# Performance work log

Measured on AMD Instinct MI355X. Metric: run time of the kernel, lower is better.

## Reference

```python
import jax, jax.numpy as jnp
import numpy as np

B, C, L = 16, 256, 2048

def setup_inputs() -> dict:
    key = jax.random.key(0)
    y = jax.random.normal(key, (B, C, L), dtype=jnp.float32)
    alpha = jnp.float32(0.5)
    beta = jnp.float32(0.5)
    gamma = jnp.float32(0.0)
    return {"y": y, "alpha": alpha, "beta": beta, "gamma": gamma}

def reference(y, alpha, beta, gamma):
    # y: [B, C, L]
    Bs, Cs, Ls = y.shape
    # channel attention: scores over channels, scaled by 1/sqrt(L)
    scale_c = 1.0 / np.sqrt(max(Ls, 1)).astype(np.float32)
    scores_c = jnp.einsum('bcl,bdl->bcd', y, y) * scale_c          # [B, C, C]
    attn_c = jax.nn.softmax(scores_c, axis=-1)
    y_c = jnp.einsum('bcd,bdl->bcl', attn_c, y)                    # [B, C, L]
    # time attention: scores over time steps, scaled by 1/sqrt(C)
    scale_t = 1.0 / np.sqrt(max(Cs, 1)).astype(np.float32)
    scores_t = jnp.einsum('bcl,bcm->blm', y, y) * scale_t          # [B, L, L]
    attn_t = jax.nn.softmax(scores_t, axis=-1)
    y_t = jnp.einsum('blm,bcm->bcl', attn_t, y)                    # [B, C, L]
    # learnable weighted combine + residual (gamma)
    out = alpha * y_c + beta * y_t + gamma * y
    return out
```

## Files before the change

kernel.cpp:

```cpp
#include <hip/hip_runtime.h>

#define B_ 16
#define C_ 256
#define L_ 2048

typedef __attribute__((ext_vector_type(8))) short short8;
typedef __attribute__((ext_vector_type(4))) float float4v;

__device__ inline float4v mfma16(short8 a, short8 b, float4v c) {
  return __builtin_amdgcn_mfma_f32_16x16x32_bf16(a, b, c, 0, 0, 0);
}

__device__ inline ushort f2bf(float x) {
  union { float f; unsigned u; } v; v.f = x;
  unsigned r = (v.u + 0x7fffu + ((v.u >> 16) & 1u)) >> 16;
  return (ushort)r;
}

__device__ inline void dma16(const ushort* g, void* l) {
  __builtin_amdgcn_global_load_lds(
      (const __attribute__((address_space(1))) unsigned int*)(g),
      (__attribute__((address_space(3))) unsigned int*)(l), 16, 0, 0);
}

#define BAR_FULL() asm volatile("s_waitcnt vmcnt(0) lgkmcnt(0)\ns_barrier" ::: "memory")
#define BAR_LGKM() asm volatile("s_waitcnt lgkmcnt(0)\ns_barrier" ::: "memory")

__global__ __launch_bounds__(256) void cvt_kernel(const float* __restrict__ y,
                                                  ushort* __restrict__ yb,
                                                  ushort* __restrict__ ytb) {
  __shared__ float tile[32][33];
  int b = blockIdx.z, ct = blockIdx.y, lt = blockIdx.x;
  int tx = threadIdx.x & 31, ty = threadIdx.x >> 5;
  size_t base = ((size_t)b * C_ + (size_t)ct * 32) * L_ + (size_t)lt * 32;
#pragma unroll
  for (int i = 0; i < 4; ++i) {
    int r = ty + i * 8;
    float v = y[base + (size_t)r * L_ + tx];
    tile[r][tx] = v;
    yb[base + (size_t)r * L_ + tx] = f2bf(v);
  }
  __syncthreads();
  size_t tbase = ((size_t)b * L_ + (size_t)lt * 32) * C_ + (size_t)ct * 32;
#pragma unroll
  for (int i = 0; i < 4; ++i) {
    int r = ty + i * 8;
    ytb[tbase + (size_t)r * C_ + tx] = f2bf(tile[tx][r]);
  }
}

__global__ __launch_bounds__(256) void pk_kernel(const ushort* __restrict__ yb,
                                                 ushort* __restrict__ Pc,
                                                 float* __restrict__ ginvW) {
  const int blk = blockIdx.x;
  const int b = (blk & 7) + 8 * ((blk >> 3) & 1);
  const int m0 = (blk >> 4) * 16;
  const int tid = threadIdx.x;
  const int w = tid >> 6, lane = tid & 63, quad = lane >> 4, l16 = lane & 15;
  const float scale = 0.022097086912079608f;
  const float SHIFT = 45.0f;

  __shared__ __align__(16) unsigned char Tb[2][32768];
  __shared__ float wsum[4][16];

  const ushort* Yb = yb + (size_t)b * C_ * L_;
  const int chq = ((lane & 3) - ((lane >> 3) & 3)) & 3;
  const int dl = (lane >> 2) * L_ + chq * 8;
  const int sK = (quad + ((l16 >> 1) & 3)) & 3;
  const int frag_lane = l16 * 64 + sK * 16;

  float4v acc[4];
#pragma unroll
  for (int nt = 0; nt < 4; ++nt) acc[nt] = (float4v){0.f, 0.f, 0.f, 0.f};

#pragma unroll
  for (int j = 0; j < 8; ++j) {
    int gi = w * 8 + j, kk2 = gi >> 4, chgrp = gi & 15;
    dma16(Yb + (size_t)chgrp * 16 * L_ + kk2 * 32 + dl, (void*)(Tb[0] + gi * 1024));
  }

  for (int c = 0; c < 32; ++c) {
    BAR_FULL();
    if (c < 31) {
      int kc = (c + 1) * 64;
      unsigned char* bp = Tb[(c + 1) & 1];
#pragma unroll
      for (int j = 0; j < 8; ++j) {
        int gi = w * 8 + j, kk2 = gi >> 4, chgrp = gi & 15;
        dma16(Yb + (size_t)chgrp * 16 * L_ + kc + kk2 * 32 + dl, (void*)(bp + gi * 1024));
      }
    }
    const unsigned char* cbuf = Tb[c & 1];
#pragma unroll
    for (int kk2 = 0; kk2 < 2; ++kk2) {
      short8 aA = *(const short8*)(cbuf + (kk2 * 16 + (m0 >> 4)) * 1024 + frag_lane);
#pragma unroll
      for (int nt = 0; nt < 4; ++nt) {
        short8 bB = *(const short8*)(cbuf + (kk2 * 16 + w * 4 + nt) * 1024 + frag_lane);
        acc[nt] = mfma16(aA, bB, acc[nt]);
      }
    }
  }

  float p[4][4], rs[4] = {0.f, 0.f, 0.f, 0.f};
#pragma unroll
  for (int nt = 0; nt < 4; ++nt)
#pragma unroll
    for (int r = 0; r < 4; ++r) {
      p[nt][r] = __expf(fmaf(acc[nt][r], scale, -SHIFT));
      rs[r] += p[nt][r];
    }
  ushort* Pb = Pc + ((size_t)b * 256 + m0) * 256;
#pragma unroll
  for (int nt = 0; nt < 4; ++nt)
#pragma unroll
    for (int r = 0; r < 4; ++r)
      Pb[(quad * 4 + r) * 256 + w * 64 + nt * 16 + l16] = f2bf(p[nt][r]);
#pragma unroll
  for (int r = 0; r < 4; ++r)
#pragma unroll
    for (int off = 1; off < 16; off <<= 1) rs[r] += __shfl_xor(rs[r], off);
  if (l16 == 0) {
#pragma unroll
    for (int r = 0; r < 4; ++r) wsum[w][quad * 4 + r] = rs[r];
  }
  __syncthreads();
  if (tid < 16)
    ginvW[b * 256 + m0 + tid] =
        1.0f / (wsum[0][tid] + wsum[1][tid] + wsum[2][tid] + wsum[3][tid]);
}

__global__ __launch_bounds__(256) void ok_kernel(
    const ushort* __restrict__ ytb, const ushort* __restrict__ Pc,
    const float* __restrict__ ginvW, const float* __restrict__ y,
    float* __restrict__ out, const float* __restrict__ alpha_p,
    const float* __restrict__ gamma_p) {
  const int blk = blockIdx.x;
  const int b = (blk & 7) + 8 * ((blk >> 3) & 1);
  const int t = blk >> 4;
  const int mq = t & 3, lt = t >> 2;
  const int tid = threadIdx.x;
  const int w = tid >> 6, lane = tid & 63, quad = lane >> 4, l16 = lane & 15;
  const int wv_m = w >> 1, wv_n = w & 1;

  __shared__ __align__(16) unsigned char Pl[32768];
  __shared__ __align__(16) unsigned char Vl[2][16384];
  __shared__ float ginvb[64];

  const ushort* Yt = ytb + (size_t)b * L_ * C_;
  const int chq = ((lane & 3) - ((lane >> 3) & 3)) & 3;
  const int sK = (quad + ((l16 >> 1) & 3)) & 3;
  const int frag_lane = l16 * 64 + sK * 16;

  const float alpha = alpha_p[0], gamma = gamma_p[0];

  const ushort* Pq = Pc + ((size_t)b * 256 + mq * 64) * 256;
#pragma unroll
  for (int j = 0; j < 8; ++j) {
    int gi = w * 8 + j, rgrp = gi >> 3, kk = gi & 7;
    dma16(Pq + (rgrp * 16 + (lane >> 2)) * 256 + kk * 32 + chq * 8,
          (void*)(Pl + gi * 1024));
  }
#pragma unroll
  for (int j = 0; j < 4; ++j) {
    int gi = w * 4 + j, pg = gi >> 3, kk = gi & 7;
    dma16(Yt + (size_t)(lt * 256 + pg * 16 + (lane >> 2)) * C_ + kk * 32 + chq * 8,
          (void*)(Vl[0] + gi * 1024));
  }
  if (tid < 64) ginvb[tid] = ginvW[b * 256 + mq * 64 + tid];

  short8 Af[2][8];
  float gvr[2][4];
#pragma unroll
  for (int c = 0; c < 8; ++c) {
    BAR_FULL();
    if (c == 0) {
#pragma unroll
      for (int mt = 0; mt < 2; ++mt) {
#pragma unroll
        for (int kk = 0; kk < 8; ++kk)
          Af[mt][kk] = *(const short8*)(Pl + ((wv_m * 2 + mt) * 8 + kk) * 1024 + frag_lane);
#pragma unroll
        for (int r = 0; r < 4; ++r)
          gvr[mt][r] = alpha * ginvb[wv_m * 32 + mt * 16 + quad * 4 + r];
      }
    }
    if (c < 7) {
      unsigned char* bp = Vl[(c + 1) & 1];
#pragma unroll
      for (int j = 0; j < 4; ++j) {
        int gi = w * 4 + j, pg = gi >> 3, kk = gi & 7;
        dma16(Yt + (size_t)(lt * 256 + (c + 1) * 32 + pg * 16 + (lane >> 2)) * C_ +
                  kk * 32 + chq * 8,
              (void*)(bp + gi * 1024));
      }
    }
    const unsigned char* vb = Vl[c & 1];
    float4v f0 = (float4v){0.f, 0.f, 0.f, 0.f};
    float4v f1 = (float4v){0.f, 0.f, 0.f, 0.f};
#pragma unroll
    for (int kk = 0; kk < 8; ++kk) {
      short8 bf = *(const short8*)(vb + (wv_n * 8 + kk) * 1024 + frag_lane);
      f0 = mfma16(Af[0][kk], bf, f0);
      f1 = mfma16(Af[1][kk], bf, f1);
    }
#pragma unroll
    for (int mt = 0; mt < 2; ++mt) {
      float4v f = mt ? f1 : f0;
#pragma unroll
      for (int r = 0; r < 4; ++r) {
        int row = mq * 64 + wv_m * 32 + mt * 16 + quad * 4 + r;
        int col = lt * 256 + c * 32 + wv_n * 16 + l16;
        size_t idx = ((size_t)b * C_ + row) * L_ + col;
        out[idx] = fmaf(gvr[mt][r], f[r], gamma * y[idx]);
      }
    }
  }
}

__global__ __launch_bounds__(256, 2) void time_kernel(
    const ushort* __restrict__ yb, const ushort* __restrict__ ytb,
    float* __restrict__ out, const float* __restrict__ beta_p) {
  const int blk = blockIdx.x;
  const int b = (blk & 7) + 8 * ((blk >> 3) & 1);
  const int m0 = (blk >> 4) * 64;
  const int tid = threadIdx.x;
  const int w = tid >> 6, lane = tid & 63, quad = lane >> 4, l16 = lane & 15;
  const int mtw = w >> 1, kt2 = w & 1;
  const float scale = 0.0625f;
  const float SHIFT = 16.0f;

  __shared__ __align__(16) unsigned char buf[2][32768];
  __shared__ ushort Pd[2][64 * 40];
  __shared__ float wsum[4][64];
  __shared__ float ginv[64];

  const ushort* Yt = ytb + (size_t)b * L_ * C_;
  const ushort* Yb = yb + (size_t)b * C_ * L_;
  const int chq = ((lane & 3) - ((lane >> 3) & 3)) & 3;
  const int klK = (lane >> 2) * C_ + chq * 8;
  const int vlV = (lane >> 2) * L_ + chq * 8;
  const int sK = (quad + ((l16 >> 1) & 3)) & 3;
  const int frag_lane = l16 * 64 + sK * 16;

  short8 Qf[2][8];
#pragma unroll
  for (int mt = 0; mt < 2; ++mt)
#pragma unroll
    for (int kk = 0; kk < 8; ++kk)
      Qf[mt][kk] = *(const short8*)(Yt + (size_t)(m0 + mtw * 32 + mt * 16 + l16) * C_ +
                                    kk * 32 + quad * 8);

  float4v facc[4][4];
#pragma unroll
  for (int mt = 0; mt < 4; ++mt)
#pragma unroll
    for (int nt = 0; nt < 4; ++nt) facc[mt][nt] = (float4v){0.f, 0.f, 0.f, 0.f};
  float rs[2][4] = {{0.f, 0.f, 0.f, 0.f}, {0.f, 0.f, 0.f, 0.f}};

#pragma unroll
  for (int j = 0; j < 8; ++j) {
    int gi = w * 8 + j;
    if (gi < 16) {
      int kk = gi >> 1, g = gi & 1;
      dma16(Yt + (size_t)(g * 16) * C_ + kk * 32 + klK, (void*)(buf[0] + gi * 1024));
    } else {
      int cg = gi - 16;
      dma16(Yb + (size_t)cg * 16 * L_ + vlV, (void*)(buf[0] + gi * 1024));
    }
  }

  for (int c = 0; c < 64; ++c) {
    const int cb = c & 1;
    BAR_FULL();
    if (c < 63) {
      const int kc = (c + 1) * 32;
      unsigned char* bp = buf[cb ^ 1];
#pragma unroll
      for (int j = 0; j < 8; ++j) {
        int gi = w * 8 + j;
        if (gi < 16) {
          int kk = gi >> 1, g = gi & 1;
          dma16(Yt + (size_t)(kc + g * 16) * C_ + kk * 32 + klK, (void*)(bp + gi * 1024));
        } else {
          int cg = gi - 16;
          dma16(Yb + (size_t)cg * 16 * L_ + kc + vlV, (void*)(bp + gi * 1024));
        }
      }
    }
    float4v s0 = (float4v){0.f, 0.f, 0.f, 0.f};
    float4v s1 = (float4v){0.f, 0.f, 0.f, 0.f};
#pragma unroll
    for (int kk = 0; kk < 8; ++kk) {
      short8 bf = *(const short8*)(buf[cb] + (kk * 2 + kt2) * 1024 + frag_lane);
      s0 = mfma16(Qf[0][kk], bf, s0);
      s1 = mfma16(Qf[1][kk], bf, s1);
    }
#pragma unroll
    for (int mt = 0; mt < 2; ++mt) {
      float4v s = mt ? s1 : s0;
#pragma unroll
      for (int r = 0; r < 4; ++r) {
        float p = __expf(fmaf(s[r], scale, -SHIFT));
        rs[mt][r] += p;
        Pd[cb][(mtw * 32 + mt * 16 + quad * 4 + r) * 40 + kt2 * 16 + l16] = f2bf(p);
      }
    }
    BAR_LGKM();
#pragma unroll
    for (int mt = 0; mt < 4; ++mt) {
      short8 va = *(const short8*)(buf[cb] + (16 + w * 4 + mt) * 1024 + frag_lane);
#pragma unroll
      for (int nt = 0; nt < 4; ++nt) {
        short8 pb = *(const short8*)(&Pd[cb][(nt * 16 + l16) * 40 + quad * 8]);
        facc[mt][nt] = mfma16(va, pb, facc[mt][nt]);
      }
    }
  }

  __syncthreads();
#pragma unroll
  for (int mt = 0; mt < 2; ++mt)
#pragma unroll
    for (int r = 0; r < 4; ++r)
#pragma unroll
      for (int off = 1; off < 16; off <<= 1) rs[mt][r] += __shfl_xor(rs[mt][r], off);
  if (l16 == 0) {
#pragma unroll
    for (int mt = 0; mt < 2; ++mt)
#pragma unroll
      for (int r = 0; r < 4; ++r)
        wsum[w][mtw * 32 + mt * 16 + quad * 4 + r] = rs[mt][r];
  }
  __syncthreads();
  if (tid < 64) {
    int mh = tid >> 5;
    ginv[tid] = 1.0f / (wsum[mh * 2][tid] + wsum[mh * 2 + 1][tid]);
  }
  __syncthreads();

  const float beta = beta_p[0];
  float gq[4];
#pragma unroll
  for (int nt = 0; nt < 4; ++nt) gq[nt] = beta * ginv[nt * 16 + l16];

#pragma unroll
  for (int mt = 0; mt < 4; ++mt)
#pragma unroll
    for (int nt = 0; nt < 4; ++nt)
#pragma unroll
      for (int r = 0; r < 4; ++r) {
        int ch = w * 64 + mt * 16 + quad * 4 + r;
        size_t idx = ((size_t)b * C_ + ch) * L_ + m0 + nt * 16 + l16;
        out[idx] = fmaf(gq[nt], facc[mt][nt][r], out[idx]);
      }
}

extern "C" void kernel_launch(void* const* d_in, const int* in_sizes, int n_in,
                              void* d_out, int out_size, void* d_ws, size_t ws_size,
                              hipStream_t stream) {
  const float* y = (const float*)d_in[0];
  const float* alpha = (const float*)d_in[1];
  const float* beta = (const float*)d_in[2];
  const float* gamma = (const float*)d_in[3];
  float* out = (float*)d_out;

  ushort* yb = (ushort*)d_ws;
  ushort* ytb = yb + (size_t)B_ * C_ * L_;
  ushort* Pc = ytb + (size_t)B_ * C_ * L_;
  float* ginvW = (float*)(Pc + (size_t)B_ * 256 * 256);

  hipLaunchKernelGGL(cvt_kernel, dim3(L_ / 32, C_ / 32, B_), dim3(256), 0, stream,
                     y, yb, ytb);
  hipLaunchKernelGGL(pk_kernel, dim3(256), dim3(256), 0, stream, yb, Pc, ginvW);
  hipLaunchKernelGGL(ok_kernel, dim3(512), dim3(256), 0, stream,
                     ytb, Pc, ginvW, y, out, alpha, gamma);
  hipLaunchKernelGGL(time_kernel, dim3(512), dim3(256), 0, stream,
                     yb, ytb, out, beta);
}
```

Baseline: 226.0 us.

## Fuse channel score and output kernels, drop Pc round-trip, single-buffer Pd

Merges pk_kernel and ok_kernel into one chan_kernel. Each block computes its 16-row channel score block, then keeps the softmax probabilities and inverse row sums in LDS and applies them straight to a 1024-column half of L. This removes the global Pc/ginvW write and re-read and one kernel launch, at the cost of computing each score block twice (once per L half). The time kernel drops its double-buffered Pd to a single buffer to save LDS. Both kernels now precompute DMA pointers and advance them by a fixed stride instead of recomputing addresses every iteration.

Result: slower. 232.6 us (+2.9%).

```diff
diff --git a/kernel.cpp b/kernel.cpp
--- a/kernel.cpp
+++ b/kernel.cpp
@@ -49,171 +49,136 @@
   }
 }
 
-__global__ __launch_bounds__(256) void pk_kernel(const ushort* __restrict__ yb,
-                                                 ushort* __restrict__ Pc,
-                                                 float* __restrict__ ginvW) {
+__global__ __launch_bounds__(256) void chan_kernel(
+    const ushort* __restrict__ yb, const ushort* __restrict__ ytb,
+    const float* __restrict__ y, float* __restrict__ out,
+    const float* __restrict__ alpha_p, const float* __restrict__ gamma_p) {
   const int blk = blockIdx.x;
   const int b = (blk & 7) + 8 * ((blk >> 3) & 1);
-  const int m0 = (blk >> 4) * 16;
+  const int rest = blk >> 4;
+  const int m0 = (rest & 15) * 16;
+  const int Lh = rest >> 4;
   const int tid = threadIdx.x;
   const int w = tid >> 6, lane = tid & 63, quad = lane >> 4, l16 = lane & 15;
   const float scale = 0.022097086912079608f;
   const float SHIFT = 45.0f;
 
   __shared__ __align__(16) unsigned char Tb[2][32768];
+  __shared__ ushort Pl[16 * 264];
   __shared__ float wsum[4][16];
+  __shared__ float ginvb[16];
 
   const ushort* Yb = yb + (size_t)b * C_ * L_;
-  const int chq = ((lane & 3) - ((lane >> 3) & 3)) & 3;
-  const int dl = (lane >> 2) * L_ + chq * 8;
-  const int sK = (quad + ((l16 >> 1) & 3)) & 3;
-  const int frag_lane = l16 * 64 + sK * 16;
-
-  float4v acc[4];
-#pragma unroll
-  for (int nt = 0; nt < 4; ++nt) acc[nt] = (float4v){0.f, 0.f, 0.f, 0.f};
-
-#pragma unroll
-  for (int j = 0; j < 8; ++j) {
-    int gi = w * 8 + j, kk2 = gi >> 4, chgrp = gi & 15;
-    dma16(Yb + (size_t)chgrp * 16 * L_ + kk2 * 32 + dl, (void*)(Tb[0] + gi * 1024));
-  }
-
-  for (int c = 0; c < 32; ++c) {
-    BAR_FULL();
-    if (c < 31) {
-      int kc = (c + 1) * 64;
-      unsigned char* bp = Tb[(c + 1) & 1];
-#pragma unroll
-      for (int j = 0; j < 8; ++j) {
-        int gi = w * 8 + j, kk2 = gi >> 4, chgrp = gi & 15;
-        dma16(Yb + (size_t)chgrp * 16 * L_ + kc + kk2 * 32 + dl, (void*)(bp + gi * 1024));
-      }
-    }
-    const unsigned char* cbuf = Tb[c & 1];
-#pragma unroll
-    for (int kk2 = 0; kk2 < 2; ++kk2) {
-      short8 aA = *(const short8*)(cbuf + (kk2 * 16 + (m0 >> 4)) * 1024 + frag_lane);
-#pragma unroll
-      for (int nt = 0; nt < 4; ++nt) {
-        short8 bB = *(const short8*)(cbuf + (kk2 * 16 + w * 4 + nt) * 1024 + frag_lane);
-        acc[nt] = mfma16(aA, bB, acc[nt]);
-      }
-    }
-  }
-
-  float p[4][4], rs[4] = {0.f, 0.f, 0.f, 0.f};
-#pragma unroll
-  for (int nt = 0; nt < 4; ++nt)
-#pragma unroll
-    for (int r = 0; r < 4; ++r) {
-      p[nt][r] = __expf(fmaf(acc[nt][r], scale, -SHIFT));
-      rs[r] += p[nt][r];
-    }
-  ushort* Pb = Pc + ((size_t)b * 256 + m0) * 256;
-#pragma unroll
-  for (int nt = 0; nt < 4; ++nt)
-#pragma unroll
-    for (int r = 0; r < 4; ++r)
-      Pb[(quad * 4 + r) * 256 + w * 64 + nt * 16 + l16] = f2bf(p[nt][r]);
-#pragma unroll
-  for (int r = 0; r < 4; ++r)
-#pragma unroll
-    for (int off = 1; off < 16; off <<= 1) rs[r] += __shfl_xor(rs[r], off);
-  if (l16 == 0) {
-#pragma unroll
-    for (int r = 0; r < 4; ++r) wsum[w][quad * 4 + r] = rs[r];
-  }
-  __syncthreads();
-  if (tid < 16)
-    ginvW[b * 256 + m0 + tid] =
-        1.0f / (wsum[0][tid] + wsum[1][tid] + wsum[2][tid] + wsum[3][tid]);
-}
-
-__global__ __launch_bounds__(256) void ok_kernel(
-    const ushort* __restrict__ ytb, const ushort* __restrict__ Pc,
-    const float* __restrict__ ginvW, const float* __restrict__ y,
-    float* __restrict__ out, const float* __restrict__ alpha_p,
-    const float* __restrict__ gamma_p) {
-  const int blk = blockIdx.x;
-  const int b = (blk & 7) + 8 * ((blk >> 3) & 1);
-  const int t = blk >> 4;
-  const int mq = t & 3, lt = t >> 2;
-  const int tid = threadIdx.x;
-  const int w = tid >> 6, lane = tid & 63, quad = lane >> 4, l16 = lane & 15;
-  const int wv_m = w >> 1, wv_n = w & 1;
-
-  __shared__ __align__(16) unsigned char Pl[32768];
-  __shared__ __align__(16) unsigned char Vl[2][16384];
-  __shared__ float ginvb[64];
-
   const ushort* Yt = ytb + (size_t)b * L_ * C_;
   const int chq = ((lane & 3) - ((lane >> 3) & 3)) & 3;
   const int sK = (quad + ((l16 >> 1) & 3)) & 3;
   const int frag_lane = l16 * 64 + sK * 16;
 
+  const ushort* ap[8];
+#pragma unroll
+  for (int j = 0; j < 8; ++j) {
+    int gi = w * 8 + j, kk2 = gi >> 4, chgrp = gi & 15;
+    ap[j] = Yb + (size_t)chgrp * 16 * L_ + kk2 * 32 + (lane >> 2) * L_ + chq * 8;
+  }
+  const ushort* vp[8];
+#pragma unroll
+  for (int j = 0; j < 8; ++j) {
+    int gi = w * 8 + j, pg = gi >> 3, kk = gi & 7;
+    vp[j] = Yt + (size_t)(Lh * 1024 + pg * 16 + (lane >> 2)) * C_ + kk * 32 + chq * 8;
+  }
+
+#pragma unroll
+  for (int j = 0; j < 8; ++j) {
+    dma16(ap[j], (void*)(Tb[0] + (w * 8 + j) * 1024));
+    ap[j] += 64;
+  }
+
+  float4v acc[4];
+#pragma unroll
+  for (int nt = 0; nt < 4; ++nt) acc[nt] = (float4v){0.f, 0.f, 0.f, 0.f};
+
+  for (int c = 0; c < 32; ++c) {
+    BAR_FULL();
+    if (c < 31) {
+      unsigned char* bp = Tb[(c + 1) & 1];
+#pragma unroll
+      for (int j = 0; j < 8; ++j) {
+        dma16(ap[j], (void*)(bp + (w * 8 + j) * 1024));
+        ap[j] += 64;
+      }
+    } else {
+#pragma unroll
+      for (int j = 0; j < 8; ++j) {
+        dma16(vp[j], (void*)(Tb[0] + (w * 8 + j) * 1024));
+        vp[j] += (size_t)64 * C_;
+      }
+    }
+    const unsigned char* cbuf = Tb[c & 1];
+#pragma unroll
+    for (int kk2 = 0; kk2 < 2; ++kk2) {
+      short8 aA = *(const short8*)(cbuf + (kk2 * 16 + (m0 >> 4)) * 1024 + frag_lane);
+#pragma unroll
+      for (int nt = 0; nt < 4; ++nt) {
+        short8 bB = *(const short8*)(cbuf + (kk2 * 16 + w * 4 + nt) * 1024 + frag_lane);
+        acc[nt] = mfma16(aA, bB, acc[nt]);
+      }
+    }
+  }
+
+  float rs[4] = {0.f, 0.f, 0.f, 0.f};
+#pragma unroll
+  for (int nt = 0; nt < 4; ++nt)
+#pragma unroll
+    for (int r = 0; r < 4; ++r) {
+      float p = __expf(fmaf(acc[nt][r], scale, -SHIFT));
+      rs[r] += p;
+      Pl[(quad * 4 + r) * 264 + w * 64 + nt * 16 + l16] = f2bf(p);
+    }
+#pragma unroll
+  for (int r = 0; r < 4; ++r)
+#pragma unroll
+    for (int off = 1; off < 16; off <<= 1) rs[r] += __shfl_xor(rs[r], off);
+  if (l16 == 0) {
+#pragma unroll
+    for (int r = 0; r < 4; ++r) wsum[w][quad * 4 + r] = rs[r];
+  }
+  __syncthreads();
+  if (tid < 16)
+    ginvb[tid] = 1.0f / (wsum[0][tid] + wsum[1][tid] + wsum[2][tid] + wsum[3][tid]);
+  __syncthreads();
+
   const float alpha = alpha_p[0], gamma = gamma_p[0];
-
-  const ushort* Pq = Pc + ((size_t)b * 256 + mq * 64) * 256;
-#pragma unroll
-  for (int j = 0; j < 8; ++j) {
-    int gi = w * 8 + j, rgrp = gi >> 3, kk = gi & 7;
-    dma16(Pq + (rgrp * 16 + (lane >> 2)) * 256 + kk * 32 + chq * 8,
-          (void*)(Pl + gi * 1024));
-  }
-#pragma unroll
-  for (int j = 0; j < 4; ++j) {
-    int gi = w * 4 + j, pg = gi >> 3, kk = gi & 7;
-    dma16(Yt + (size_t)(lt * 256 + pg * 16 + (lane >> 2)) * C_ + kk * 32 + chq * 8,
-          (void*)(Vl[0] + gi * 1024));
-  }
-  if (tid < 64) ginvb[tid] = ginvW[b * 256 + mq * 64 + tid];
-
-  short8 Af[2][8];
-  float gvr[2][4];
-#pragma unroll
-  for (int c = 0; c < 8; ++c) {
+  short8 Af[8];
+#pragma unroll
+  for (int ks = 0; ks < 8; ++ks)
+    Af[ks] = *(const short8*)(&Pl[l16 * 264 + ks * 32 + quad * 8]);
+  float gvr[4];
+#pragma unroll
+  for (int r = 0; r < 4; ++r) gvr[r] = alpha * ginvb[quad * 4 + r];
+
+  for (int cb = 0; cb < 16; ++cb) {
     BAR_FULL();
-    if (c == 0) {
-#pragma unroll
-      for (int mt = 0; mt < 2; ++mt) {
-#pragma unroll
-        for (int kk = 0; kk < 8; ++kk)
-          Af[mt][kk] = *(const short8*)(Pl + ((wv_m * 2 + mt) * 8 + kk) * 1024 + frag_lane);
-#pragma unroll
-        for (int r = 0; r < 4; ++r)
-          gvr[mt][r] = alpha * ginvb[wv_m * 32 + mt * 16 + quad * 4 + r];
-      }
-    }
-    if (c < 7) {
-      unsigned char* bp = Vl[(c + 1) & 1];
-#pragma unroll
-      for (int j = 0; j < 4; ++j) {
-        int gi = w * 4 + j, pg = gi >> 3, kk = gi & 7;
-        dma16(Yt + (size_t)(lt * 256 + (c + 1) * 32 + pg * 16 + (lane >> 2)) * C_ +
-                  kk * 32 + chq * 8,
-              (void*)(bp + gi * 1024));
-      }
-    }
-    const unsigned char* vb = Vl[c & 1];
-    float4v f0 = (float4v){0.f, 0.f, 0.f, 0.f};
-    float4v f1 = (float4v){0.f, 0.f, 0.f, 0.f};
+    if (cb < 15) {
+      unsigned char* bp = Tb[(cb + 1) & 1];
+#pragma unroll
+      for (int j = 0; j < 8; ++j) {
+        dma16(vp[j], (void*)(bp + (w * 8 + j) * 1024));
+        vp[j] += (size_t)64 * C_;
+      }
+    }
+    const unsigned char* vb = Tb[cb & 1];
+    float4v f = (float4v){0.f, 0.f, 0.f, 0.f};
 #pragma unroll
     for (int kk = 0; kk < 8; ++kk) {
-      short8 bf = *(const short8*)(vb + (wv_n * 8 + kk) * 1024 + frag_lane);
-      f0 = mfma16(Af[0][kk], bf, f0);
-      f1 = mfma16(Af[1][kk], bf, f1);
-    }
-#pragma unroll
-    for (int mt = 0; mt < 2; ++mt) {
-      float4v f = mt ? f1 : f0;
-#pragma unroll
-      for (int r = 0; r < 4; ++r) {
-        int row = mq * 64 + wv_m * 32 + mt * 16 + quad * 4 + r;
-        int col = lt * 256 + c * 32 + wv_n * 16 + l16;
-        size_t idx = ((size_t)b * C_ + row) * L_ + col;
-        out[idx] = fmaf(gvr[mt][r], f[r], gamma * y[idx]);
-      }
+      short8 bf = *(const short8*)(vb + (w * 8 + kk) * 1024 + frag_lane);
+      f = mfma16(Af[kk], bf, f);
+    }
+    int col = Lh * 1024 + cb * 64 + w * 16 + l16;
+#pragma unroll
+    for (int r = 0; r < 4; ++r) {
+      int row = m0 + quad * 4 + r;
+      size_t idx = ((size_t)b * C_ + row) * L_ + col;
+      out[idx] = fmaf(gvr[r], f[r], gamma * y[idx]);
     }
   }
 }
@@ -231,7 +196,7 @@
   const float SHIFT = 16.0f;
 
   __shared__ __align__(16) unsigned char buf[2][32768];
-  __shared__ ushort Pd[2][64 * 40];
+  __shared__ ushort Pd[64 * 40];
   __shared__ float wsum[4][64];
   __shared__ float ginv[64];
 
@@ -251,41 +216,42 @@
       Qf[mt][kk] = *(const short8*)(Yt + (size_t)(m0 + mtw * 32 + mt * 16 + l16) * C_ +
                                     kk * 32 + quad * 8);
 
-  float4v facc[4][4];
-#pragma unroll
-  for (int mt = 0; mt < 4; ++mt)
-#pragma unroll
-    for (int nt = 0; nt < 4; ++nt) facc[mt][nt] = (float4v){0.f, 0.f, 0.f, 0.f};
-  float rs[2][4] = {{0.f, 0.f, 0.f, 0.f}, {0.f, 0.f, 0.f, 0.f}};
-
+  const ushort* dp[8];
 #pragma unroll
   for (int j = 0; j < 8; ++j) {
     int gi = w * 8 + j;
     if (gi < 16) {
       int kk = gi >> 1, g = gi & 1;
-      dma16(Yt + (size_t)(g * 16) * C_ + kk * 32 + klK, (void*)(buf[0] + gi * 1024));
+      dp[j] = Yt + (size_t)(g * 16) * C_ + kk * 32 + klK;
     } else {
       int cg = gi - 16;
-      dma16(Yb + (size_t)cg * 16 * L_ + vlV, (void*)(buf[0] + gi * 1024));
-    }
+      dp[j] = Yb + (size_t)cg * 16 * L_ + vlV;
+    }
+  }
+  const int dstride = (w < 2) ? 32 * C_ : 32;
+
+  float4v facc[4][4];
+#pragma unroll
+  for (int mt = 0; mt < 4; ++mt)
+#pragma unroll
+    for (int nt = 0; nt < 4; ++nt) facc[mt][nt] = (float4v){0.f, 0.f, 0.f, 0.f};
+  float rs[2][4] = {{0.f, 0.f, 0.f, 0.f}, {0.f, 0.f, 0.f, 0.f}};
+
+#pragma unroll
+  for (int j = 0; j < 8; ++j) {
+    dma16(dp[j], (void*)(buf[0] + (w * 8 + j) * 1024));
+    dp[j] += dstride;
   }
 
   for (int c = 0; c < 64; ++c) {
     const int cb = c & 1;
     BAR_FULL();
     if (c < 63) {
-      const int kc = (c + 1) * 32;
       unsigned char* bp = buf[cb ^ 1];
 #pragma unroll
       for (int j = 0; j < 8; ++j) {
-        int gi = w * 8 + j;
-        if (gi < 16) {
-          int kk = gi >> 1, g = gi & 1;
-          dma16(Yt + (size_t)(kc + g * 16) * C_ + kk * 32 + klK, (void*)(bp + gi * 1024));
-        } else {
-          int cg = gi - 16;
-          dma16(Yb + (size_t)cg * 16 * L_ + kc + vlV, (void*)(bp + gi * 1024));
-        }
+        dma16(dp[j], (void*)(bp + (w * 8 + j) * 1024));
+        dp[j] += dstride;
       }
     }
     float4v s0 = (float4v){0.f, 0.f, 0.f, 0.f};
@@ -303,7 +269,7 @@
       for (int r = 0; r < 4; ++r) {
         float p = __expf(fmaf(s[r], scale, -SHIFT));
         rs[mt][r] += p;
-        Pd[cb][(mtw * 32 + mt * 16 + quad * 4 + r) * 40 + kt2 * 16 + l16] = f2bf(p);
+        Pd[(mtw * 32 + mt * 16 + quad * 4 + r) * 40 + kt2 * 16 + l16] = f2bf(p);
       }
     }
     BAR_LGKM();
@@ -312,7 +278,7 @@
       short8 va = *(const short8*)(buf[cb] + (16 + w * 4 + mt) * 1024 + frag_lane);
 #pragma unroll
       for (int nt = 0; nt < 4; ++nt) {
-        short8 pb = *(const short8*)(&Pd[cb][(nt * 16 + l16) * 40 + quad * 8]);
+        short8 pb = *(const short8*)(&Pd[(nt * 16 + l16) * 40 + quad * 8]);
         facc[mt][nt] = mfma16(va, pb, facc[mt][nt]);
       }
     }
@@ -367,14 +333,11 @@
 
   ushort* yb = (ushort*)d_ws;
   ushort* ytb = yb + (size_t)B_ * C_ * L_;
-  ushort* Pc = ytb + (size_t)B_ * C_ * L_;
-  float* ginvW = (float*)(Pc + (size_t)B_ * 256 * 256);
 
   hipLaunchKernelGGL(cvt_kernel, dim3(L_ / 32, C_ / 32, B_), dim3(256), 0, stream,
                      y, yb, ytb);
-  hipLaunchKernelGGL(pk_kernel, dim3(256), dim3(256), 0, stream, yb, Pc, ginvW);
-  hipLaunchKernelGGL(ok_kernel, dim3(512), dim3(256), 0, stream,
-                     ytb, Pc, ginvW, y, out, alpha, gamma);
+  hipLaunchKernelGGL(chan_kernel, dim3(512), dim3(256), 0, stream,
+                     yb, ytb, y, out, alpha, gamma);
   hipLaunchKernelGGL(time_kernel, dim3(512), dim3(256), 0, stream,
                      yb, ytb, out, beta);
 }
```
